# Kernel optimization log

Measured on AMD Instinct MI355X. Metric: run time of the kernel, lower is better.

## Reference

```python
import jax, jax.numpy as jnp
import numpy as np

D_MODEL, N_STATE, E_INNER, K_CONV, DT_RANK = 1024, 16, 2048, 4, 64
EPS = 1e-6

def _silu(x):
    return x * jax.nn.sigmoid(x)

def _rmsnorm(x, w):
    var = jnp.mean(x * x, axis=-1, keepdims=True)
    return x * jax.lax.rsqrt(var + EPS) * w

def _causal_dwconv(x, conv_w):
    # x: [B, L, E]; conv_w: [E, 1, K] depthwise kernel
    xc = jnp.swapaxes(x, 1, 2)  # [B, E, L]
    xc = jnp.pad(xc, ((0, 0), (0, 0), (K_CONV - 1, 0)))
    y = jax.lax.conv_general_dilated(
        xc, conv_w, window_strides=(1,), padding='VALID',
        dimension_numbers=('NCL', 'OIL', 'NCL'), feature_group_count=E_INNER)
    return jnp.swapaxes(y, 1, 2)  # [B, L, E]

def _selective_scan(u, delta, A, Bm, Cm, Dp):
    # u, delta: [B, L, E]; Bm, Cm: [B, L, N]; A: [E, N]; Dp: [E]
    def step(h, inp):
        d_t, B_t, C_t, u_t = inp  # [B,E], [B,N], [B,N], [B,E]
        dA = jnp.exp(d_t[..., None] * A)                       # [B,E,N]
        h = dA * h + (d_t * u_t)[..., None] * B_t[:, None, :]  # [B,E,N]
        y = jnp.einsum('ben,bn->be', h, C_t)
        return h, y
    h0 = jnp.zeros((u.shape[0], E_INNER, N_STATE), u.dtype)
    xs = (jnp.swapaxes(delta, 0, 1), jnp.swapaxes(Bm, 0, 1),
          jnp.swapaxes(Cm, 0, 1), jnp.swapaxes(u, 0, 1))
    h_last, ys = jax.lax.scan(step, h0, xs)
    return jnp.swapaxes(ys, 0, 1) + u * Dp, h_last

def setup_inputs() -> dict:
    key = jax.random.key(0)
    ks = jax.random.split(key, 8)
    B, L = 4, 1024
    hidden_states = jax.random.normal(ks[0], (B, L, D_MODEL), jnp.float32)
    norm_w = jnp.ones((D_MODEL,), jnp.float32)
    W_in = jax.random.normal(ks[1], (D_MODEL, 2 * E_INNER), jnp.float32) * (D_MODEL ** -0.5)
    conv_w = jax.random.normal(ks[2], (E_INNER, 1, K_CONV), jnp.float32) * (K_CONV ** -0.5)
    W_x = jax.random.normal(ks[3], (E_INNER, DT_RANK + 2 * N_STATE), jnp.float32) * (E_INNER ** -0.5)
    W_dt = jax.random.normal(ks[4], (DT_RANK, E_INNER), jnp.float32) * (DT_RANK ** -0.5)
    # dt bias so softplus(b) lands roughly in [delta_min, delta_max]
    dt = jnp.exp(jax.random.uniform(ks[5], (E_INNER,)) * (np.log(0.1) - np.log(0.001)) + np.log(0.001))
    b_dt = dt + jnp.log(-jnp.expm1(-dt))  # inverse softplus
    A_log = jnp.log(jnp.broadcast_to(jnp.arange(1, N_STATE + 1, dtype=jnp.float32), (E_INNER, N_STATE)))
    D_param = jnp.ones((E_INNER,), jnp.float32)
    W_out = jax.random.normal(ks[6], (E_INNER, D_MODEL), jnp.float32) * (E_INNER ** -0.5)
    return {"hidden_states": hidden_states, "norm_w": norm_w, "W_in": W_in,
            "conv_w": conv_w, "W_x": W_x, "W_dt": W_dt, "b_dt": b_dt,
            "A_log": A_log, "D_param": D_param, "W_out": W_out}

def reference(hidden_states, norm_w, W_in, conv_w, W_x, W_dt, b_dt, A_log, D_param, W_out):
    residual = hidden_states
    x = _rmsnorm(hidden_states, norm_w)
    xz = jnp.einsum('bld,de->ble', x, W_in)          # [B,L,2E]
    x_in, z = jnp.split(xz, 2, axis=-1)
    x_act = _silu(_causal_dwconv(x_in, conv_w))      # [B,L,E]
    x_db = jnp.einsum('ble,er->blr', x_act, W_x)     # [B,L,R+2N]
    dt_lr = x_db[..., :DT_RANK]
    Bm = x_db[..., DT_RANK:DT_RANK + N_STATE]
    Cm = x_db[..., DT_RANK + N_STATE:]
    delta = jax.nn.softplus(jnp.einsum('blr,re->ble', dt_lr, W_dt) + b_dt)
    A = -jnp.exp(A_log)
    y, h_last = _selective_scan(x_act, delta, A, Bm, Cm, D_param)
    y = y * _silu(z)
    out = jnp.einsum('ble,ed->bld', y, W_out)
    # dropout is identity in eval mode
    return residual + out, h_last
```

## Files before the change

kernel.cpp:

```cpp
#include <hip/hip_runtime.h>
#include <cstdint>
#include <cstddef>

#define DM 1024
#define EI 2048
#define NS 16
#define DR 64
#define BB 4
#define LL 1024
#define MM (BB*LL)
#define NCHUNK 32
#define CHUNK 32

typedef __attribute__((ext_vector_type(8))) __bf16 bf16x8;
typedef __attribute__((ext_vector_type(4))) float f32x4;
typedef __attribute__((ext_vector_type(8))) unsigned short u16x8;

__device__ __forceinline__ unsigned short f2bf(float f) {
    union { float f; unsigned int u; } v; v.f = f;
    unsigned int r = v.u + 0x7FFFu + ((v.u >> 16) & 1u);
    return (unsigned short)(r >> 16);
}
__device__ __forceinline__ float bf2f(unsigned short u) {
    union { unsigned int u; float f; } v; v.u = ((unsigned int)u) << 16;
    return v.f;
}

__device__ __forceinline__ void gload_lds16(const unsigned short* g, unsigned short* l) {
    __builtin_amdgcn_global_load_lds(
        (const __attribute__((address_space(1))) unsigned int*)g,
        (__attribute__((address_space(3))) unsigned int*)l, 16, 0, 0);
}

__global__ void rmsnorm_bf16(const float* __restrict__ x, const float* __restrict__ w,
                             unsigned short* __restrict__ out) {
    int m = blockIdx.x, tid = threadIdx.x;
    const float4* row = (const float4*)(x + (size_t)m * DM);
    float4 v = row[tid];
    float ss = v.x*v.x + v.y*v.y + v.z*v.z + v.w*v.w;
    #pragma unroll
    for (int o = 32; o; o >>= 1) ss += __shfl_down(ss, o);
    __shared__ float red[4];
    if ((tid & 63) == 0) red[tid >> 6] = ss;
    __syncthreads();
    ss = red[0] + red[1] + red[2] + red[3];
    float scale = rsqrtf(ss * (1.0f / DM) + 1e-6f);
    const float4* wr = (const float4*)w;
    float4 wv = wr[tid];
    ushort4 o4;
    o4.x = f2bf(v.x * scale * wv.x);
    o4.y = f2bf(v.y * scale * wv.y);
    o4.z = f2bf(v.z * scale * wv.z);
    o4.w = f2bf(v.w * scale * wv.w);
    ((ushort4*)out)[(size_t)m * (DM/4) + tid] = o4;
}

__global__ void transpose_all(const float* __restrict__ W_in, const float* __restrict__ W_x,
                              const float* __restrict__ W_dt, const float* __restrict__ W_out,
                              unsigned short* __restrict__ wt_in, unsigned short* __restrict__ wt_x,
                              unsigned short* __restrict__ wt_dt, unsigned short* __restrict__ wt_out) {
    __shared__ float t[32][33];
    int id = blockIdx.x;
    const float* in; unsigned short* out;
    int R, C, Cpad, bx, by;
    if (id < 4096)      { in = W_in;  out = wt_in;  R = 1024; C = 4096; Cpad = 4096; bx = id & 127; by = id >> 7; }
    else if (id < 4352) { id -= 4096; in = W_x;  out = wt_x;  R = 2048; C = 96;  Cpad = 128;  bx = id & 3;  by = id >> 2; }
    else if (id < 4480) { id -= 4352; in = W_dt; out = wt_dt; R = 64;   C = 2048; Cpad = 2048; bx = id & 63; by = id >> 6; }
    else                { id -= 4480; in = W_out; out = wt_out; R = 2048; C = 1024; Cpad = 1024; bx = id & 31; by = id >> 5; }
    int c0 = bx * 32, r0 = by * 32;
    int tx = threadIdx.x, ty = threadIdx.y;
    #pragma unroll
    for (int j = 0; j < 32; j += 8) {
        int r = r0 + ty + j, c = c0 + tx;
        t[ty + j][tx] = (r < R && c < C) ? in[(size_t)r * C + c] : 0.f;
    }
    __syncthreads();
    #pragma unroll
    for (int j = 0; j < 32; j += 8) {
        int c = c0 + ty + j, r = r0 + tx;
        if (c < Cpad && r < R) out[(size_t)c * R + r] = f2bf(t[tx][ty + j]);
    }
}

__global__ __launch_bounds__(512, 2)
void gemm256_8ph(const unsigned short* __restrict__ A,
                 const unsigned short* __restrict__ Bt,
                 unsigned short* __restrict__ C) {
    __shared__ __attribute__((aligned(16))) unsigned short lds[65536];
    const int tid = threadIdx.x;
    const int w = tid >> 6, lane = tid & 63;
    const int wm = w >> 2, wn = w & 3;
    const int m0 = blockIdx.y * 256, n0 = blockIdx.x * 256;
    const int r = lane & 15;
    const int psl = ((lane >> 4) ^ ((lane >> 1) & 3)) * 8;
    const int aoff = (wm * 128 + r) * 32 + psl;
    const int boff = (wn * 64 + r) * 32 + psl;
    const int c0 = w * 2;
    const int srow = lane >> 2;
    const int scol = ((lane & 3) ^ ((lane >> 3) & 3)) * 8;

    f32x4 acc[8][4];
    f32x4 zero = {0.f, 0.f, 0.f, 0.f};
    #pragma unroll
    for (int i = 0; i < 8; ++i)
        #pragma unroll
        for (int j = 0; j < 4; ++j) acc[i][j] = zero;

    auto stage = [&](const unsigned short* __restrict__ G, int row0, int mat, int t, int ks) {
        const unsigned short* g = G + (size_t)(row0 + c0 * 16 + srow) * 1024 + t * 64 + ks * 32 + scol;
        unsigned short* l = lds + (t & 1) * 32768 + mat * 16384 + ks * 8192 + c0 * 512;
        gload_lds16(g, l);
        gload_lds16(g + 16 * 1024, l + 512);
    };

    stage(Bt, n0, 1, 0, 0); stage(A, m0, 0, 0, 0);
    stage(Bt, n0, 1, 0, 1); stage(A, m0, 0, 0, 1);
    stage(Bt, n0, 1, 1, 0); stage(A, m0, 0, 1, 0);
    stage(Bt, n0, 1, 1, 1);
    asm volatile("s_waitcnt vmcnt(6)" ::: "memory");
    __builtin_amdgcn_s_barrier();
    asm volatile("" ::: "memory");

    for (int t = 0; t < 16; ++t) {
        const unsigned short* la = lds + (t & 1) * 32768;
        const unsigned short* lb = la + 16384;
        bf16x8 af[4], bq[4];

        #pragma unroll
        for (int i = 0; i < 4; ++i) af[i] = *(const bf16x8*)(la + aoff + i * 512);
        #pragma unroll
        for (int j = 0; j < 4; ++j) bq[j] = *(const bf16x8*)(lb + boff + j * 512);
        if (t + 1 < 16) stage(A, m0, 0, t + 1, 1);
        __builtin_amdgcn_s_barrier();
        asm volatile("" ::: "memory");
        __builtin_amdgcn_s_setprio(1);
        #pragma unroll
        for (int i = 0; i < 4; ++i)
            #pragma unroll
            for (int j = 0; j < 4; ++j)
                acc[i][j] = __builtin_amdgcn_mfma_f32_16x16x32_bf16(af[i], bq[j], acc[i][j], 0, 0, 0);
        __builtin_amdgcn_s_setprio(0);
        __builtin_amdgcn_s_barrier();
        asm volatile("" ::: "memory");

        #pragma unroll
        for (int i = 0; i < 4; ++i) af[i] = *(const bf16x8*)(la + aoff + (4 + i) * 512);
        if (t + 2 < 16) stage(Bt, n0, 1, t + 2, 0);
        __builtin_amdgcn_s_barrier();
        asm volatile("" ::: "memory");
        __builtin_amdgcn_s_setprio(1);
        #pragma unroll
        for (int i = 0; i < 4; ++i)
            #pragma unroll
            for (int j = 0; j < 4; ++j)
                acc[4 + i][j] = __builtin_amdgcn_mfma_f32_16x16x32_bf16(af[i], bq[j], acc[4 + i][j], 0, 0, 0);
        __builtin_amdgcn_s_setprio(0);
        __builtin_amdgcn_s_barrier();
        asm volatile("" ::: "memory");

        #pragma unroll
        for (int i = 0; i < 4; ++i) af[i] = *(const bf16x8*)(la + 8192 + aoff + i * 512);
        #pragma unroll
        for (int j = 0; j < 4; ++j) bq[j] = *(const bf16x8*)(lb + 8192 + boff + j * 512);
        if (t + 2 < 16) stage(A, m0, 0, t + 2, 0);
        __builtin_amdgcn_s_barrier();
        asm volatile("" ::: "memory");
        __builtin_amdgcn_s_setprio(1);
        #pragma unroll
        for (int i = 0; i < 4; ++i)
            #pragma unroll
            for (int j = 0; j < 4; ++j)
                acc[i][j] = __builtin_amdgcn_mfma_f32_16x16x32_bf16(af[i], bq[j], acc[i][j], 0, 0, 0);
        __builtin_amdgcn_s_setprio(0);
        __builtin_amdgcn_s_barrier();
        asm volatile("" ::: "memory");

        #pragma unroll
        for (int i = 0; i < 4; ++i) af[i] = *(const bf16x8*)(la + 8192 + aoff + (4 + i) * 512);
        if (t + 2 < 16) stage(Bt, n0, 1, t + 2, 1);
        __builtin_amdgcn_s_barrier();
        asm volatile("" ::: "memory");
        __builtin_amdgcn_s_setprio(1);
        #pragma unroll
        for (int i = 0; i < 4; ++i)
            #pragma unroll
            for (int j = 0; j < 4; ++j)
                acc[4 + i][j] = __builtin_amdgcn_mfma_f32_16x16x32_bf16(af[i], bq[j], acc[4 + i][j], 0, 0, 0);
        __builtin_amdgcn_s_setprio(0);
        if (t + 2 < 16) { asm volatile("s_waitcnt vmcnt(6)" ::: "memory"); }
        else            { asm volatile("s_waitcnt vmcnt(0)" ::: "memory"); }
        __builtin_amdgcn_s_barrier();
        asm volatile("" ::: "memory");
    }

    const int q4 = (lane >> 4) * 4;
    #pragma unroll
    for (int mi = 0; mi < 8; ++mi) {
        #pragma unroll
        for (int nj = 0; nj < 4; ++nj) {
            int gm = m0 + wm * 128 + mi * 16 + q4;
            int gn = n0 + wn * 64 + nj * 16 + r;
            #pragma unroll
            for (int tt = 0; tt < 4; ++tt)
                C[(size_t)(gm + tt) * 4096 + gn] = f2bf(acc[mi][nj][tt]);
        }
    }
}

template<int EPI>
__global__ void gemm_mfma(const unsigned short* __restrict__ A,
                          const unsigned short* __restrict__ Bt,
                          float* __restrict__ C,
                          const float* __restrict__ ex1,
                          unsigned short* __restrict__ exb,
                          int M, int N, int K, int ldc) {
    __shared__ __attribute__((aligned(16))) unsigned short lds_a[128 * 32];
    __shared__ __attribute__((aligned(16))) unsigned short lds_b[128 * 32];
    const int tid = threadIdx.x;
    const int w = tid >> 6, lane = tid & 63;
    const int m0 = blockIdx.y * 128;
    const int n0 = (EPI == 3) ? 0 : blockIdx.x * 128;
    const int kstart = (EPI == 3) ? blockIdx.x * (K >> 3) : 0;
    const int kend   = (EPI == 3) ? kstart + (K >> 3) : K;
    const int wm = (w & 1) * 64, wn = (w >> 1) * 64;
    const int q = lane >> 4, r = lane & 15;
    const int srow = lane >> 2;
    const int scol = (lane & 3) * 8;

    f32x4 acc[4][4];
    f32x4 zero = {0.f, 0.f, 0.f, 0.f};
    #pragma unroll
    for (int i = 0; i < 4; ++i)
        #pragma unroll
        for (int j = 0; j < 4; ++j) acc[i][j] = zero;

    for (int kb = kstart; kb < kend; kb += 32) {
        __syncthreads();
        #pragma unroll
        for (int j = 0; j < 2; ++j) {
            int rbase = w * 32 + j * 16;
            gload_lds16(A  + (size_t)(m0 + rbase + srow) * K + kb + scol, lds_a + rbase * 32);
            gload_lds16(Bt + (size_t)(n0 + rbase + srow) * K + kb + scol, lds_b + rbase * 32);
        }
        __syncthreads();
        bf16x8 af[4], bfr[4];
        #pragma unroll
        for (int mi = 0; mi < 4; ++mi)
            af[mi] = *(const bf16x8*)(lds_a + (wm + mi * 16 + r) * 32 + q * 8);
        #pragma unroll
        for (int ni = 0; ni < 4; ++ni)
            bfr[ni] = *(const bf16x8*)(lds_b + (wn + ni * 16 + r) * 32 + q * 8);
        #pragma unroll
        for (int mi = 0; mi < 4; ++mi)
            #pragma unroll
            for (int ni = 0; ni < 4; ++ni)
                acc[mi][ni] = __builtin_amdgcn_mfma_f32_16x16x32_bf16(af[mi], bfr[ni], acc[mi][ni], 0, 0, 0);
    }

    #pragma unroll
    for (int mi = 0; mi < 4; ++mi) {
        #pragma unroll
        for (int ni = 0; ni < 4; ++ni) {
            f32x4 v = acc[mi][ni];
            int gmb = m0 + wm + mi * 16 + q * 4;
            int gn  = n0 + wn + ni * 16 + r;
            #pragma unroll
            for (int t = 0; t < 4; ++t) {
                int gm = gmb + t;
                float val = v[t];
                if (EPI == 1) {
                    C[(size_t)gm * ldc + gn] = val + ex1[(size_t)gm * ldc + gn];
                } else if (EPI == 2) {
                    val += ex1[gn];
                    val = fmaxf(val, 0.f) + log1pf(__expf(-fabsf(val)));
                    exb[(size_t)gm * ldc + gn] = f2bf(val);
                } else if (EPI == 3) {
                    C[((size_t)blockIdx.x * M + gm) * 128 + gn] = val;
                } else {
                    exb[(size_t)gm * ldc + gn] = f2bf(val);
                }
            }
        }
    }
}

__global__ void xproj_reduce(const float* __restrict__ Pp,
                             unsigned short* __restrict__ dtlr, float* __restrict__ bc) {
    int id = blockIdx.x * 256 + threadIdx.x;
    int n = id & 127, m = id >> 7;
    if (n >= DR + 2 * NS) return;
    float s = 0.f;
    #pragma unroll
    for (int ks = 0; ks < 8; ++ks)
        s += Pp[((size_t)ks * MM + m) * 128 + n];
    if (n < DR) dtlr[(size_t)m * DR + n] = f2bf(s);
    else bc[(size_t)m * 32 + (n - DR)] = s;
}

__global__ void conv_silu8(const unsigned short* __restrict__ xzb, const float* __restrict__ cw,
                           unsigned short* __restrict__ xab) {
    size_t idx8 = ((size_t)blockIdx.x * 256 + threadIdx.x) * 8;
    int e = (int)(idx8 & (EI - 1));
    size_t m = idx8 >> 11;
    int l = (int)(m & (LL - 1));
    u16x8 x0 = *(const u16x8*)(xzb + m * 4096 + e);
    u16x8 zer = {0,0,0,0,0,0,0,0};
    u16x8 x1 = (l >= 1) ? *(const u16x8*)(xzb + (m - 1) * 4096 + e) : zer;
    u16x8 x2 = (l >= 2) ? *(const u16x8*)(xzb + (m - 2) * 4096 + e) : zer;
    u16x8 x3 = (l >= 3) ? *(const u16x8*)(xzb + (m - 3) * 4096 + e) : zer;
    u16x8 o;
    #pragma unroll
    for (int j = 0; j < 8; ++j) {
        float4 wv = ((const float4*)cw)[e + j];
        float s = bf2f(x0[j]) * wv.w + bf2f(x1[j]) * wv.z
                + bf2f(x2[j]) * wv.y + bf2f(x3[j]) * wv.x;
        float a = s / (1.f + __expf(-s));
        o[j] = f2bf(a);
    }
    *(u16x8*)(xab + idx8) = o;
}

__global__ void scan_phase1(const unsigned short* __restrict__ dbufb, const unsigned short* __restrict__ xu,
                            const float* __restrict__ bc, const float* __restrict__ A_log,
                            float* __restrict__ P, float* __restrict__ H) {
    int e = blockIdx.x * 256 + threadIdx.x;
    int c = blockIdx.y, b = blockIdx.z;
    float A[NS], h[NS], p[NS];
    #pragma unroll
    for (int n = 0; n < NS; ++n) {
        A[n] = -expf(A_log[(size_t)e * NS + n]);
        h[n] = 0.f; p[n] = 1.f;
    }
    int mbase = b * LL + c * CHUNK;
    for (int t = 0; t < CHUNK; ++t) {
        size_t m = (size_t)(mbase + t);
        float d = bf2f(dbufb[m * 2048 + e]);
        float u = bf2f(xu[m * 2048 + e]);
        float du = d * u;
        const float* Bv = bc + m * 32;
        #pragma unroll
        for (int n = 0; n < NS; ++n) {
            float dA = __expf(d * A[n]);
            p[n] *= dA;
            h[n] = fmaf(dA, h[n], du * Bv[n]);
        }
    }
    size_t base = ((size_t)(b * NCHUNK + c) * NS) * 2048 + e;
    #pragma unroll
    for (int n = 0; n < NS; ++n) {
        P[base + (size_t)n * 2048] = p[n];
        H[base + (size_t)n * 2048] = h[n];
    }
}

__global__ void scan_phase2(const float* __restrict__ P, const float* __restrict__ H,
                            float* __restrict__ h0, float* __restrict__ hlast) {
    int id = blockIdx.x * 256 + threadIdx.x;
    int e = id & (EI - 1);
    int bn = id >> 11;
    int n = bn & (NS - 1), b = bn >> 4;
    float h = 0.f;
    #pragma unroll
    for (int c = 0; c < NCHUNK; ++c) {
        size_t ix = (((size_t)(b * NCHUNK + c) * NS) + n) * 2048 + e;
        h0[ix] = h;
        h = fmaf(P[ix], h, H[ix]);
    }
    hlast[(((size_t)b * EI + e) * NS) + n] = h;
}

__global__ void scan_phase3(const unsigned short* __restrict__ dbufb, const unsigned short* __restrict__ xu,
                            const unsigned short* __restrict__ xzb,
                            const float* __restrict__ bc, const float* __restrict__ A_log,
                            const float* __restrict__ Dp, const float* __restrict__ h0,
                            unsigned short* __restrict__ ybf) {
    int e = blockIdx.x * 256 + threadIdx.x;
    int c = blockIdx.y, b = blockIdx.z;
    float A[NS], h[NS];
    size_t base = ((size_t)(b * NCHUNK + c) * NS) * 2048 + e;
    #pragma unroll
    for (int n = 0; n < NS; ++n) {
        A[n] = -expf(A_log[(size_t)e * NS + n]);
        h[n] = h0[base + (size_t)n * 2048];
    }
    float D = Dp[e];
    int mbase = b * LL + c * CHUNK;
    for (int t = 0; t < CHUNK; ++t) {
        size_t m = (size_t)(mbase + t);
        float d = bf2f(dbufb[m * 2048 + e]);
        float u = bf2f(xu[m * 2048 + e]);
        float du = d * u;
        const float* Bv = bc + m * 32;
        float y = 0.f;
        #pragma unroll
        for (int n = 0; n < NS; ++n) {
            float dA = __expf(d * A[n]);
            h[n] = fmaf(dA, h[n], du * Bv[n]);
            y = fmaf(h[n], Bv[16 + n], y);
        }
        y = fmaf(u, D, y);
        float z = bf2f(xzb[m * 4096 + 2048 + e]);
        float sil = z / (1.f + __expf(-z));
        ybf[m * 2048 + e] = f2bf(y * sil);
    }
}

extern "C" void kernel_launch(void* const* d_in, const int* in_sizes, int n_in,
                              void* d_out, int out_size, void* d_ws, size_t ws_size,
                              hipStream_t stream) {
    (void)in_sizes; (void)n_in; (void)out_size; (void)ws_size;
    const float* hidden = (const float*)d_in[0];
    const float* norm_w = (const float*)d_in[1];
    const float* W_in   = (const float*)d_in[2];
    const float* conv_w = (const float*)d_in[3];
    const float* W_x    = (const float*)d_in[4];
    const float* W_dt   = (const float*)d_in[5];
    const float* b_dt   = (const float*)d_in[6];
    const float* A_log  = (const float*)d_in[7];
    const float* D_par  = (const float*)d_in[8];
    const float* W_out  = (const float*)d_in[9];
    float* out = (float*)d_out;
    char* ws = (char*)d_ws;
    const size_t MB = 1ull << 20;

    unsigned short* xzb      = (unsigned short*)(ws + 0);
    unsigned short* xact_bf  = (unsigned short*)(ws + 32 * MB);
    unsigned short* xnorm_bf = (unsigned short*)(ws + 48 * MB);
    unsigned short* wt_in    = (unsigned short*)(ws + 56 * MB);
    unsigned short* wt_out   = (unsigned short*)(ws + 64 * MB);
    unsigned short* wt_x     = (unsigned short*)(ws + 68 * MB);
    unsigned short* wt_dt    = (unsigned short*)(ws + 68 * MB + 512 * 1024);
    unsigned short* dtlr     = (unsigned short*)(ws + 69 * MB);
    float*          bc       = (float*)(ws + 69 * MB + 512 * 1024);
    unsigned short* dbufb    = (unsigned short*)(ws + 70 * MB);
    unsigned short* ybf      = (unsigned short*)(ws + 86 * MB);
    float*          h0       = (float*)(ws + 102 * MB);
    float*          P        = (float*)(ws + 118 * MB);
    float*          Hb       = (float*)(ws + 134 * MB);
    float* Ppart = P;
    float* hlast = out + (size_t)MM * DM;

    rmsnorm_bf16<<<MM, 256, 0, stream>>>(hidden, norm_w, xnorm_bf);
    transpose_all<<<6528, dim3(32, 8), 0, stream>>>(W_in, W_x, W_dt, W_out,
                                                    wt_in, wt_x, wt_dt, wt_out);

    gemm256_8ph<<<dim3(16, 16), 512, 0, stream>>>(xnorm_bf, wt_in, xzb);
    conv_silu8<<<(MM * EI) / (256 * 8), 256, 0, stream>>>(xzb, conv_w, xact_bf);
    gemm_mfma<3><<<dim3(8, 32), 256, 0, stream>>>(xact_bf, wt_x, Ppart, nullptr, nullptr,
                                                  MM, 128, 2048, 128);
    xproj_reduce<<<(MM * 128) / 256, 256, 0, stream>>>(Ppart, dtlr, bc);
    gemm_mfma<2><<<dim3(16, 32), 256, 0, stream>>>(dtlr, wt_dt, nullptr, b_dt, dbufb,
                                                   MM, 2048, 64, 2048);
    scan_phase1<<<dim3(8, NCHUNK, BB), 256, 0, stream>>>(dbufb, xact_bf, bc, A_log, P, Hb);
    scan_phase2<<<(BB * NS * EI) / 256, 256, 0, stream>>>(P, Hb, h0, hlast);
    scan_phase3<<<dim3(8, NCHUNK, BB), 256, 0, stream>>>(dbufb, xact_bf, xzb, bc, A_log, D_par, h0, ybf);
    gemm_mfma<1><<<dim3(8, 32), 256, 0, stream>>>(ybf, wt_out, out, hidden, nullptr,
                                                  MM, 1024, 2048, 1024);
}
```

Measured before the change: 325.5 us.

## Triple-buffer gemm_mfma with async LDS prefetch, XOR swizzle and 64-wide K tiles

Rewrites the main loop of the generic MFMA GEMM. The K tile grows from 32 to 64, and LDS becomes a ring of three buffers (one for EPI==2). Global-to-LDS loads run two tiles ahead, gated by vmcnt waits and a single barrier per iteration instead of two. LDS rows use an XOR swizzle to avoid bank conflicts, MFMA sections run at raised wave priority, and the EPI==1 block order is remapped for better L2 locality. The goal is to hide global load latency and cut sync overhead, at the cost of more LDS per block and so possibly lower occupancy.

```diff
diff --git a/kernel.cpp b/kernel.cpp
--- a/kernel.cpp
+++ b/kernel.cpp
@@ -214,18 +214,25 @@
                           const float* __restrict__ ex1,
                           unsigned short* __restrict__ exb,
                           int M, int N, int K, int ldc) {
-    __shared__ __attribute__((aligned(16))) unsigned short lds_a[128 * 32];
-    __shared__ __attribute__((aligned(16))) unsigned short lds_b[128 * 32];
+    constexpr int NBUF = (EPI == 2) ? 1 : 3;
+    __shared__ __attribute__((aligned(16))) unsigned short lds[NBUF * 16384];
     const int tid = threadIdx.x;
     const int w = tid >> 6, lane = tid & 63;
-    const int m0 = blockIdx.y * 128;
-    const int n0 = (EPI == 3) ? 0 : blockIdx.x * 128;
-    const int kstart = (EPI == 3) ? blockIdx.x * (K >> 3) : 0;
+    int bx = blockIdx.x, by = blockIdx.y;
+    if (EPI == 1) {
+        int orig = bx + 8 * by;
+        int nl = (orig & 7) * 32 + (orig >> 3);
+        bx = nl & 7; by = nl >> 3;
+    }
+    const int m0 = by * 128;
+    const int n0 = (EPI == 3) ? 0 : bx * 128;
+    const int kstart = (EPI == 3) ? bx * (K >> 3) : 0;
     const int kend   = (EPI == 3) ? kstart + (K >> 3) : K;
+    const int nt = (kend - kstart) >> 6;
     const int wm = (w & 1) * 64, wn = (w >> 1) * 64;
     const int q = lane >> 4, r = lane & 15;
-    const int srow = lane >> 2;
-    const int scol = (lane & 3) * 8;
+    const int srow8 = lane >> 3;
+    const int sslot = (lane & 7) ^ (lane >> 3);
 
     f32x4 acc[4][4];
     f32x4 zero = {0.f, 0.f, 0.f, 0.f};
@@ -234,27 +241,64 @@
         #pragma unroll
         for (int j = 0; j < 4; ++j) acc[i][j] = zero;
 
-    for (int kb = kstart; kb < kend; kb += 32) {
-        __syncthreads();
-        #pragma unroll
-        for (int j = 0; j < 2; ++j) {
-            int rbase = w * 32 + j * 16;
-            gload_lds16(A  + (size_t)(m0 + rbase + srow) * K + kb + scol, lds_a + rbase * 32);
-            gload_lds16(Bt + (size_t)(n0 + rbase + srow) * K + kb + scol, lds_b + rbase * 32);
-        }
-        __syncthreads();
-        bf16x8 af[4], bfr[4];
-        #pragma unroll
-        for (int mi = 0; mi < 4; ++mi)
-            af[mi] = *(const bf16x8*)(lds_a + (wm + mi * 16 + r) * 32 + q * 8);
-        #pragma unroll
-        for (int ni = 0; ni < 4; ++ni)
-            bfr[ni] = *(const bf16x8*)(lds_b + (wn + ni * 16 + r) * 32 + q * 8);
-        #pragma unroll
-        for (int mi = 0; mi < 4; ++mi)
-            #pragma unroll
-            for (int ni = 0; ni < 4; ++ni)
-                acc[mi][ni] = __builtin_amdgcn_mfma_f32_16x16x32_bf16(af[mi], bfr[ni], acc[mi][ni], 0, 0, 0);
+    auto stage = [&](int bsel, int kb) {
+        unsigned short* la = lds + bsel * 16384;
+        unsigned short* lb = la + 8192;
+        const unsigned short* ga = A  + (size_t)(m0 + w * 32 + srow8) * K + kb + sslot * 8;
+        const unsigned short* gb = Bt + (size_t)(n0 + w * 32 + srow8) * K + kb + sslot * 8;
+        #pragma unroll
+        for (int i = 0; i < 4; ++i) {
+            gload_lds16(ga + (size_t)i * 8 * K, la + (w * 4 + i) * 512);
+            gload_lds16(gb + (size_t)i * 8 * K, lb + (w * 4 + i) * 512);
+        }
+    };
+
+    stage(0, kstart);
+    if (nt > 1) {
+        stage(1, kstart + 64);
+        asm volatile("s_waitcnt vmcnt(8)" ::: "memory");
+    } else {
+        asm volatile("s_waitcnt vmcnt(0)" ::: "memory");
+    }
+    __builtin_amdgcn_s_barrier();
+    asm volatile("" ::: "memory");
+
+    int bsel = 0;
+    for (int t = 0; t < nt; ++t) {
+        if (t + 2 < nt) {
+            int b2 = bsel + 2; if (b2 >= NBUF) b2 -= NBUF;
+            stage(b2, kstart + (t + 2) * 64);
+        }
+        const unsigned short* la = lds + bsel * 16384;
+        const unsigned short* lb = la + 8192;
+        bf16x8 af[2][4], bq[2][4];
+        #pragma unroll
+        for (int ks = 0; ks < 2; ++ks) {
+            #pragma unroll
+            for (int mi = 0; mi < 4; ++mi) {
+                int arow = wm + mi * 16 + r;
+                af[ks][mi] = *(const bf16x8*)(la + arow * 64 + (((ks << 2) + q) ^ (arow & 7)) * 8);
+            }
+            #pragma unroll
+            for (int nj = 0; nj < 4; ++nj) {
+                int brow = wn + nj * 16 + r;
+                bq[ks][nj] = *(const bf16x8*)(lb + brow * 64 + (((ks << 2) + q) ^ (brow & 7)) * 8);
+            }
+        }
+        __builtin_amdgcn_s_setprio(1);
+        #pragma unroll
+        for (int ks = 0; ks < 2; ++ks)
+            #pragma unroll
+            for (int mi = 0; mi < 4; ++mi)
+                #pragma unroll
+                for (int nj = 0; nj < 4; ++nj)
+                    acc[mi][nj] = __builtin_amdgcn_mfma_f32_16x16x32_bf16(af[ks][mi], bq[ks][nj], acc[mi][nj], 0, 0, 0);
+        __builtin_amdgcn_s_setprio(0);
+        if (t + 2 < nt) { asm volatile("s_waitcnt vmcnt(8)" ::: "memory"); }
+        else            { asm volatile("s_waitcnt vmcnt(0)" ::: "memory"); }
+        __builtin_amdgcn_s_barrier();
+        asm volatile("" ::: "memory");
+        bsel = (bsel + 1 == NBUF) ? 0 : bsel + 1;
     }
 
     #pragma unroll
@@ -275,7 +319,7 @@
                     val = fmaxf(val, 0.f) + log1pf(__expf(-fabsf(val)));
                     exb[(size_t)gm * ldc + gn] = f2bf(val);
                 } else if (EPI == 3) {
-                    C[((size_t)blockIdx.x * M + gm) * 128 + gn] = val;
+                    C[((size_t)bx * M + gm) * 128 + gn] = val;
                 } else {
                     exb[(size_t)gm * ldc + gn] = f2bf(val);
                 }
```

New measurement: 422.5 us. 1.3x slower.
